# Kernel tuning notes

Measured on AMD Instinct MI355X. Metric: run time of the kernel, lower is better.

## Reference

```python
import jax, jax.numpy as jnp
import numpy as np

F8_MAX = 448.0   # max representable magnitude of float8_e4m3fn
EPS = 1e-12      # amax clamp from the source


def setup_inputs() -> dict:
    key = jax.random.key(0)
    kx, kw, kb = jax.random.split(key, 3)
    B, S, K, N = 8, 8192, 1024, 1024
    x = jax.random.normal(kx, (B, S, K), dtype=jnp.float32)
    weight = jax.random.normal(kw, (N, K), dtype=jnp.float32) * 0.02  # (out, in) like nn.Linear
    bias = jax.random.normal(kb, (N,), dtype=jnp.float32)
    return {"x": x, "weight": weight, "bias": bias}


def _quantize_fp8(t):
    """Per-tensor dynamic fp8-e4m3 quantization: returns (t_fp8, scale)."""
    scale = jnp.maximum(jnp.max(jnp.abs(t)), EPS) / F8_MAX
    t8 = (t / scale).astype(jnp.float8_e4m3fn)
    return t8, scale


def reference(x, weight, bias):
    lead = x.shape[:-1]
    K = x.shape[-1]
    N = weight.shape[0]
    x_flat = x.reshape(-1, K).astype(jnp.float32)

    # dynamic activation quantization (forward-time, per tensor)
    x8, x_scale = _quantize_fp8(x_flat)
    # weight quantization (from_linear, per tensor)
    w8, w_scale = _quantize_fp8(weight.astype(jnp.float32))

    out = jnp.dot(x8.astype(jnp.float32), w8.astype(jnp.float32).T) * (x_scale * w_scale)
    out = out.astype(x.dtype).reshape(*lead, N)
    return out + bias
```

## Files before the change

### kernel.cpp

```cpp
#include <hip/hip_runtime.h>
#include <stdint.h>

#define F8MAX 448.0f
#define QEPS 1e-12f
#define SCL_ONE 0x7F7F7F7F
#define AXB 4096

typedef float floatx16 __attribute__((ext_vector_type(16)));
typedef int   intx4    __attribute__((ext_vector_type(4)));
typedef int   intx8    __attribute__((ext_vector_type(8)));

__global__ __launch_bounds__(256) void amax_partial_xw(
    const float* __restrict__ x, int nx4,
    const float* __restrict__ w, int nw4,
    float* __restrict__ px, float* __restrict__ pw)
{
    const float4* x4 = (const float4*)x;
    const float4* w4 = (const float4*)w;
    int tid = blockIdx.x * 256 + threadIdx.x;
    int stride = gridDim.x * 256;
    float mx = 0.f, mw = 0.f;
    for (int i = tid; i < nx4; i += stride) {
        float4 v = x4[i];
        mx = fmaxf(mx, fmaxf(fmaxf(fabsf(v.x), fabsf(v.y)), fmaxf(fabsf(v.z), fabsf(v.w))));
    }
    for (int i = tid; i < nw4; i += stride) {
        float4 v = w4[i];
        mw = fmaxf(mw, fmaxf(fmaxf(fabsf(v.x), fabsf(v.y)), fmaxf(fabsf(v.z), fabsf(v.w))));
    }
    #pragma unroll
    for (int off = 32; off > 0; off >>= 1) {
        mx = fmaxf(mx, __shfl_xor(mx, off, 64));
        mw = fmaxf(mw, __shfl_xor(mw, off, 64));
    }
    __shared__ float smx[4], smw[4];
    if ((threadIdx.x & 63) == 0) { smx[threadIdx.x >> 6] = mx; smw[threadIdx.x >> 6] = mw; }
    __syncthreads();
    if (threadIdx.x == 0) {
        px[blockIdx.x] = fmaxf(fmaxf(smx[0], smx[1]), fmaxf(smx[2], smx[3]));
        pw[blockIdx.x] = fmaxf(fmaxf(smw[0], smw[1]), fmaxf(smw[2], smw[3]));
    }
}

__device__ __forceinline__ void quant_tile(const float* __restrict__ in, uint8_t* __restrict__ out,
                                           int tile, float rs, int nkt, int K)
{
    int p  = tile / nkt;
    int kt = tile - p * nkt;
    uint8_t* dst = out + (size_t)tile * 8192;
    #pragma unroll
    for (int i = 0; i < 2; i++) {
        int idx = threadIdx.x + i * 256;
        int h  = idx >> 8;
        int pc = (idx >> 7) & 1;
        int r  = idx & 127;
        const float* src = in + (size_t)(p * 128 + r) * K + kt * 64 + h * 32 + pc * 16;
        float4 f0 = *(const float4*)(src);
        float4 f1 = *(const float4*)(src + 4);
        float4 f2 = *(const float4*)(src + 8);
        float4 f3 = *(const float4*)(src + 12);
        int w0 = 0, w1 = 0, w2 = 0, w3 = 0;
        w0 = __builtin_amdgcn_cvt_pk_fp8_f32(f0.x * rs, f0.y * rs, w0, false);
        w0 = __builtin_amdgcn_cvt_pk_fp8_f32(f0.z * rs, f0.w * rs, w0, true);
        w1 = __builtin_amdgcn_cvt_pk_fp8_f32(f1.x * rs, f1.y * rs, w1, false);
        w1 = __builtin_amdgcn_cvt_pk_fp8_f32(f1.z * rs, f1.w * rs, w1, true);
        w2 = __builtin_amdgcn_cvt_pk_fp8_f32(f2.x * rs, f2.y * rs, w2, false);
        w2 = __builtin_amdgcn_cvt_pk_fp8_f32(f2.z * rs, f2.w * rs, w2, true);
        w3 = __builtin_amdgcn_cvt_pk_fp8_f32(f3.x * rs, f3.y * rs, w3, false);
        w3 = __builtin_amdgcn_cvt_pk_fp8_f32(f3.z * rs, f3.w * rs, w3, true);
        int4 rv; rv.x = w0; rv.y = w1; rv.z = w2; rv.w = w3;
        *(int4*)(dst + (size_t)idx * 16) = rv;
    }
}

__global__ __launch_bounds__(256) void quant_fused(
    const float* __restrict__ x, const float* __restrict__ w,
    uint8_t* __restrict__ x8, uint8_t* __restrict__ w8,
    const float* __restrict__ px, const float* __restrict__ pw,
    unsigned* __restrict__ hdr, int ntx, int nkt, int K)
{
    int bid = blockIdx.x;
    bool isw = (bid < 128);
    const float* par = isw ? pw : px;

    float m = 0.f;
    for (int i = threadIdx.x; i < AXB; i += 256) m = fmaxf(m, par[i]);
    #pragma unroll
    for (int off = 32; off > 0; off >>= 1) m = fmaxf(m, __shfl_xor(m, off, 64));
    __shared__ float red[4];
    if ((threadIdx.x & 63) == 0) red[threadIdx.x >> 6] = m;
    __syncthreads();
    float amax = fmaxf(fmaxf(red[0], red[1]), fmaxf(red[2], red[3]));

    float scale = fmaxf(amax, QEPS) / F8MAX;
    float rs = 1.0f / scale;

    if (threadIdx.x == 0) {
        if (bid == 0)   hdr[1] = __float_as_uint(amax);
        if (bid == 128) hdr[0] = __float_as_uint(amax);
    }

    if (isw) quant_tile(w, w8, bid, rs, nkt, K);
    else     quant_tile(x, x8, ntx - 1 - (bid - 128), rs, nkt, K);
}

__global__ __launch_bounds__(512, 1) void gemm_fp8_mx(
    const uint8_t* __restrict__ A8, const uint8_t* __restrict__ B8,
    float* __restrict__ C, const float* __restrict__ bias,
    const unsigned* __restrict__ hdr, int N, int nkt, int nbn)
{
    __shared__ uint8_t lsA[3 * 16384];
    __shared__ uint8_t lsB[3 * 16384];

    int nwg = gridDim.x;
    int bid = blockIdx.x;
    if ((nwg & 7) == 0) {
        int chunk = nwg >> 3;
        bid = (blockIdx.x & 7) * chunk + (blockIdx.x >> 3);
    }
    int bm = bid / nbn, bn = bid - bm * nbn;

    int t = threadIdx.x;
    int wave = t >> 6, lane = t & 63;
    int wr = wave >> 2, wc = wave & 3;
    int hl = lane >> 5, l31 = lane & 31;

    const uint8_t* gsrc0; const uint8_t* gsrc1; const uint8_t* gsrc2; const uint8_t* gsrc3;
    uint32_t ld0, ld1, ld2, ld3;
    bool isA = (wave < 4);
    {
        int c0 = wave * 4;
        #pragma unroll
        for (int p = 0; p < 4; p++) {
            int c = c0 + p;
            const uint8_t* g;
            uint32_t l;
            if (c < 16) {
                int h = c >> 3, sub = c & 7;
                g = A8 + (size_t)(bm * 2 + h) * nkt * 8192 + sub * 1024 + lane * 16;
                l = (uint32_t)c * 1024;
            } else {
                int cc = c - 16, h = cc >> 3, sub = cc & 7;
                g = B8 + (size_t)(bn * 2 + h) * nkt * 8192 + sub * 1024 + lane * 16;
                l = (uint32_t)cc * 1024;
            }
            if (p == 0) { gsrc0 = g; ld0 = l; }
            else if (p == 1) { gsrc1 = g; ld1 = l; }
            else if (p == 2) { gsrc2 = g; ld2 = l; }
            else { gsrc3 = g; ld3 = l; }
        }
    }
    uint8_t* lsbase = isA ? lsA : lsB;

#define ISSUE(GP, LO, KT2, B2)                                                   \
    __builtin_amdgcn_global_load_lds(                                            \
        (const __attribute__((address_space(1))) void*)((GP) + (size_t)(KT2) * 8192), \
        (__attribute__((address_space(3))) void*)(lsbase + (B2) * 16384 + (LO)), \
        16, 0, 0)

    const uint8_t* baseA = lsA + wr * 8192 + hl * 4096 + l31 * 16;
    const uint8_t* baseB = lsB + (wc >> 1) * 8192 + hl * 4096 + (wc & 1) * 1024 + l31 * 16;

    floatx16 acc[4][2];
    #pragma unroll
    for (int m = 0; m < 4; m++)
        #pragma unroll
        for (int n = 0; n < 2; n++)
            acc[m][n] = (floatx16)(0.0f);

#define RD8(BASE, OFF) __builtin_shufflevector(                         \
        *(const intx4*)((BASE) + (OFF)),                                \
        *(const intx4*)((BASE) + (OFF) + 2048), 0, 1, 2, 3, 4, 5, 6, 7)

#define MMX(m, n) acc[m][n] = __builtin_amdgcn_mfma_scale_f32_32x32x64_f8f6f4( \
        af[m], bf[n], acc[m][n], 0, 0, 0, SCL_ONE, 0, SCL_ONE)

    ISSUE(gsrc0, ld0, 0, 0); ISSUE(gsrc1, ld1, 0, 0); ISSUE(gsrc2, ld2, 0, 0); ISSUE(gsrc3, ld3, 0, 0);
    ISSUE(gsrc0, ld0, 1, 1); ISSUE(gsrc1, ld1, 1, 1); ISSUE(gsrc2, ld2, 1, 1); ISSUE(gsrc3, ld3, 1, 1);
    asm volatile("s_waitcnt vmcnt(4)" ::: "memory");
    asm volatile("s_barrier" ::: "memory");

    int cur = 0;
    for (int kt = 0; kt < nkt; kt++) {
        bool pf = (kt + 2 < nkt);
        int ib = cur - 1; if (ib < 0) ib += 3;
        const uint8_t* cA = baseA + cur * 16384;
        const uint8_t* cB = baseB + cur * 16384;
        intx8 af[4], bf[2];

        if (pf) { ISSUE(gsrc0, ld0, kt + 2, ib); ISSUE(gsrc1, ld1, kt + 2, ib);
                  ISSUE(gsrc2, ld2, kt + 2, ib); ISSUE(gsrc3, ld3, kt + 2, ib); }

        af[0] = RD8(cA, 0);    af[1] = RD8(cA, 512);
        bf[0] = RD8(cB, 0);    bf[1] = RD8(cB, 512);
        af[2] = RD8(cA, 1024); af[3] = RD8(cA, 1536);

        __builtin_amdgcn_s_setprio(1);
        MMX(0, 0); MMX(0, 1); MMX(1, 0); MMX(1, 1);
        MMX(2, 0); MMX(2, 1); MMX(3, 0); MMX(3, 1);
        __builtin_amdgcn_s_setprio(0);

        if (kt + 1 < nkt) {
            if (pf) asm volatile("s_waitcnt vmcnt(4)" ::: "memory");
            else    asm volatile("s_waitcnt vmcnt(0)" ::: "memory");
            asm volatile("s_barrier" ::: "memory");
        }
        cur++; if (cur == 3) cur = 0;
    }

    float sxv = fmaxf(__uint_as_float(hdr[0]), QEPS) / F8MAX;
    float swv = fmaxf(__uint_as_float(hdr[1]), QEPS) / F8MAX;
    float s = sxv * swv;

    #pragma unroll
    for (int m = 0; m < 4; m++) {
        int row0 = bm * 256 + wr * 128 + m * 32 + 4 * hl;
        #pragma unroll
        for (int n = 0; n < 2; n++) {
            int col = bn * 256 + wc * 64 + n * 32 + l31;
            float bv = bias[col];
            #pragma unroll
            for (int reg = 0; reg < 16; reg++) {
                int row = row0 + (reg & 3) + 8 * (reg >> 2);
                __builtin_nontemporal_store(acc[m][n][reg] * s + bv, &C[(size_t)row * N + col]);
            }
        }
    }
#undef ISSUE
#undef RD8
#undef MMX
}

extern "C" void kernel_launch(void* const* d_in, const int* in_sizes, int n_in,
                              void* d_out, int out_size, void* d_ws, size_t ws_size,
                              hipStream_t stream)
{
    const float* x    = (const float*)d_in[0];
    const float* w    = (const float*)d_in[1];
    const float* bias = (const float*)d_in[2];
    float* out = (float*)d_out;

    int N = in_sizes[2];
    int K = in_sizes[1] / N;
    int M = in_sizes[0] / K;
    int nx = in_sizes[0];
    int nw = in_sizes[1];
    int nkt = K / 64;

    uint8_t* ws = (uint8_t*)d_ws;
    unsigned* hdr = (unsigned*)ws;
    float* px = (float*)(ws + 64);
    float* pw = (float*)(ws + 64 + 16384);
    uint8_t* w8 = ws + 65536;
    uint8_t* x8 = ws + 65536 + (size_t)N * K;

    int ntx = (M / 128) * nkt;
    int ntw = (N / 128) * nkt;

    amax_partial_xw<<<AXB, 256, 0, stream>>>(x, nx / 4, w, nw / 4, px, pw);
    quant_fused<<<ntw + ntx, 256, 0, stream>>>(x, w, x8, w8, px, pw, hdr, ntx, nkt, K);

    int nbm = M / 256, nbn = N / 256;
    gemm_fp8_mx<<<nbm * nbn, 512, 0, stream>>>(x8, w8, out, bias, hdr, N, nkt, nbn);
}
```

Baseline: 219.8 us.

## Quantize full 64-row slabs via swizzled LDS transpose for coalesced loads

The quantize kernel now has each block handle a half-tile of 64 rows across the full K dimension instead of one 128x64 tile. Rows are read with fully coalesced float4 loads, converted to fp8, staged in a 64KB XOR-swizzled LDS buffer, then written out in the tiled layout the GEMM expects. The aim is to replace strided, partially coalesced global reads with contiguous row reads and fewer, larger blocks. In exchange, 64KB of LDS per block caps occupancy, and the grid shrinks from thousands of blocks to about a thousand.

```diff
diff --git a/kernel.cpp b/kernel.cpp
--- a/kernel.cpp
+++ b/kernel.cpp
@@ -42,45 +42,16 @@
     }
 }
 
-__device__ __forceinline__ void quant_tile(const float* __restrict__ in, uint8_t* __restrict__ out,
-                                           int tile, float rs, int nkt, int K)
-{
-    int p  = tile / nkt;
-    int kt = tile - p * nkt;
-    uint8_t* dst = out + (size_t)tile * 8192;
-    #pragma unroll
-    for (int i = 0; i < 2; i++) {
-        int idx = threadIdx.x + i * 256;
-        int h  = idx >> 8;
-        int pc = (idx >> 7) & 1;
-        int r  = idx & 127;
-        const float* src = in + (size_t)(p * 128 + r) * K + kt * 64 + h * 32 + pc * 16;
-        float4 f0 = *(const float4*)(src);
-        float4 f1 = *(const float4*)(src + 4);
-        float4 f2 = *(const float4*)(src + 8);
-        float4 f3 = *(const float4*)(src + 12);
-        int w0 = 0, w1 = 0, w2 = 0, w3 = 0;
-        w0 = __builtin_amdgcn_cvt_pk_fp8_f32(f0.x * rs, f0.y * rs, w0, false);
-        w0 = __builtin_amdgcn_cvt_pk_fp8_f32(f0.z * rs, f0.w * rs, w0, true);
-        w1 = __builtin_amdgcn_cvt_pk_fp8_f32(f1.x * rs, f1.y * rs, w1, false);
-        w1 = __builtin_amdgcn_cvt_pk_fp8_f32(f1.z * rs, f1.w * rs, w1, true);
-        w2 = __builtin_amdgcn_cvt_pk_fp8_f32(f2.x * rs, f2.y * rs, w2, false);
-        w2 = __builtin_amdgcn_cvt_pk_fp8_f32(f2.z * rs, f2.w * rs, w2, true);
-        w3 = __builtin_amdgcn_cvt_pk_fp8_f32(f3.x * rs, f3.y * rs, w3, false);
-        w3 = __builtin_amdgcn_cvt_pk_fp8_f32(f3.z * rs, f3.w * rs, w3, true);
-        int4 rv; rv.x = w0; rv.y = w1; rv.z = w2; rv.w = w3;
-        *(int4*)(dst + (size_t)idx * 16) = rv;
-    }
-}
-
 __global__ __launch_bounds__(256) void quant_fused(
     const float* __restrict__ x, const float* __restrict__ w,
     uint8_t* __restrict__ x8, uint8_t* __restrict__ w8,
     const float* __restrict__ px, const float* __restrict__ pw,
-    unsigned* __restrict__ hdr, int ntx, int nkt, int K)
-{
+    unsigned* __restrict__ hdr, int nhx, int nkt, int K)
+{
+    __shared__ uint8_t lds[65536];
+
     int bid = blockIdx.x;
-    bool isw = (bid < 128);
+    bool isw = (bid < 16);
     const float* par = isw ? pw : px;
 
     float m = 0.f;
@@ -96,12 +67,46 @@
     float rs = 1.0f / scale;
 
     if (threadIdx.x == 0) {
-        if (bid == 0)   hdr[1] = __float_as_uint(amax);
-        if (bid == 128) hdr[0] = __float_as_uint(amax);
-    }
-
-    if (isw) quant_tile(w, w8, bid, rs, nkt, K);
-    else     quant_tile(x, x8, ntx - 1 - (bid - 128), rs, nkt, K);
+        if (bid == 0)  hdr[1] = __float_as_uint(amax);
+        if (bid == 16) hdr[0] = __float_as_uint(amax);
+    }
+
+    int hp = isw ? bid : (nhx - 1 - (bid - 16));
+    const float* src = isw ? w : x;
+    uint8_t* dst8 = isw ? w8 : x8;
+    int p = hp >> 1, half = hp & 1;
+
+    int wave = threadIdx.x >> 6, lane = threadIdx.x & 63;
+    int K4 = K >> 2;
+
+    const float4* s4 = (const float4*)src + (size_t)(p * 128 + half * 64) * K4;
+    uint32_t key = (lane >> 2) & 7;
+    uint32_t lbase = ((uint32_t)(lane >> 4) * 4096) + (((lane >> 2) & 3) * 1024) + ((lane & 3) * 4);
+    for (int rr = 0; rr < 16; rr++) {
+        int r = rr * 4 + wave;
+        const float4* rowp = s4 + (size_t)r * K4;
+        #pragma unroll
+        for (int j = 0; j < 4; j++) {
+            float4 f = rowp[j * 64 + lane];
+            int wd = 0;
+            wd = __builtin_amdgcn_cvt_pk_fp8_f32(f.x * rs, f.y * rs, wd, false);
+            wd = __builtin_amdgcn_cvt_pk_fp8_f32(f.z * rs, f.w * rs, wd, true);
+            uint32_t a = (uint32_t)j * 16384 + lbase + (uint32_t)r * 16;
+            a ^= (key << 4);
+            *(int*)(lds + a) = wd;
+        }
+    }
+    __syncthreads();
+
+    uint8_t* outb = dst8 + (size_t)(p * nkt) * 8192 + half * 1024;
+    for (int i = 0; i < 16; i++) {
+        int c = i * 4 + wave;
+        int kt = c >> 2, hpc = c & 3;
+        uint32_t k2 = (uint32_t)(((kt & 1) << 2) | hpc);
+        uint32_t a = (uint32_t)c * 1024 + (((uint32_t)lane * 16) ^ (k2 << 4));
+        int4 v = *(const int4*)(lds + a);
+        *(int4*)(outb + (size_t)kt * 8192 + hpc * 2048 + lane * 16) = v;
+    }
 }
 
 __global__ __launch_bounds__(512, 1) void gemm_fp8_mx(
@@ -254,11 +259,11 @@
     uint8_t* w8 = ws + 65536;
     uint8_t* x8 = ws + 65536 + (size_t)N * K;
 
-    int ntx = (M / 128) * nkt;
-    int ntw = (N / 128) * nkt;
+    int nhx = (M / 128) * 2;
+    int nhw = (N / 128) * 2;
 
     amax_partial_xw<<<AXB, 256, 0, stream>>>(x, nx / 4, w, nw / 4, px, pw);
-    quant_fused<<<ntw + ntx, 256, 0, stream>>>(x, w, x8, w8, px, pw, hdr, ntx, nkt, K);
+    quant_fused<<<nhw + nhx, 256, 0, stream>>>(x, w, x8, w8, px, pw, hdr, nhx, nkt, K);
 
     int nbm = M / 256, nbn = N / 256;
     gemm_fp8_mx<<<nbm * nbn, 512, 0, stream>>>(x8, w8, out, bias, hdr, N, nkt, nbn);
```

New measurement: 219.2 us. About the same (-0.3%).
